# Performance work log

Measured on AMD Instinct MI355X. Metric: run time of the kernel, lower is better.

## Reference

```python
import jax, jax.numpy as jnp
import numpy as np

TAU = 2.0   # spikingjelly LIFNode default tau
VTH = 1.0   # config.vthreshold

@jax.custom_vjp
def atan_spike(x):
    # heaviside forward, ATan surrogate backward (spikingjelly surrogate.ATan, alpha=2)
    return (x >= 0).astype(x.dtype)

def _atan_fwd(x):
    return atan_spike(x), x

def _atan_bwd(x, g):
    alpha = 2.0
    return (g * (alpha / 2.0) / (1.0 + (jnp.pi / 2.0 * alpha * x) ** 2),)

atan_spike.defvjp(_atan_fwd, _atan_bwd)

def layer_norm(x, eps=1e-6):
    m = jnp.mean(x, axis=-1, keepdims=True)
    v = jnp.mean((x - m) ** 2, axis=-1, keepdims=True)
    return (x - m) * jax.lax.rsqrt(v + eps)

def time_shift(x):
    # ZeroPad2d((0,0,1,-1)): xx[:, t] = x[:, t-1], xx[:, 0] = 0
    return jnp.pad(x, ((0, 0), (1, 0), (0, 0)))[:, :-1]

def lif_multistep(x4):
    # spikingjelly LIFNode, step_mode='m', decay_input=True, hard reset to v_reset=0
    def step(v, xt):
        v = v + (xt - v) / TAU
        s = atan_spike(v - VTH)
        return v * (1.0 - s), s
    _, spikes = jax.lax.scan(step, jnp.zeros_like(x4[0]), x4)
    return spikes

def wkv(w, u, k, v):
    # RWKV-v4 numerically-stable WKV scan. w: [C] (negative), u: [C], k,v: [B,T,C]
    B, T, C = k.shape
    def step(carry, kv):
        aa, bb, pp = carry
        kt, vt = kv
        ww = u + kt
        p = jnp.maximum(pp, ww)
        e1 = jnp.exp(pp - p); e2 = jnp.exp(ww - p)
        y = (e1 * aa + e2 * vt) / (e1 * bb + e2)
        ww2 = pp + w
        p2 = jnp.maximum(ww2, kt)
        f1 = jnp.exp(ww2 - p2); f2 = jnp.exp(kt - p2)
        return (f1 * aa + f2 * vt, f1 * bb + f2, p2), y
    init = (jnp.zeros((B, C), k.dtype), jnp.zeros((B, C), k.dtype),
            jnp.full((B, C), -1e38, k.dtype))
    _, ys = jax.lax.scan(step, init, (jnp.moveaxis(k, 1, 0), jnp.moveaxis(v, 1, 0)))
    return jnp.moveaxis(ys, 0, 1)

def time_mix(h, time_decay, time_first, tmk, tmv, tmr, Wk, Wv, Wr, Wo):
    xx = time_shift(h)
    xk = h * tmk + xx * (1 - tmk)
    xv = h * tmv + xx * (1 - tmv)
    xr = h * tmr + xx * (1 - tmr)
    k = jnp.einsum('btc,oc->bto', xk, Wk)
    v = jnp.einsum('btc,oc->bto', xv, Wv)
    sr = jax.nn.sigmoid(jnp.einsum('btc,oc->bto', xr, Wr))
    y = wkv(-jnp.exp(time_decay), time_first, k, v)
    return jnp.einsum('btc,oc->bto', sr * y, Wo)

def channel_mix(h, cmk, cmr, Wck, Wcv, Wcr):
    xx = time_shift(h)
    xk = h * cmk + xx * (1 - cmk)
    xr = h * cmr + xx * (1 - cmr)
    k = jnp.square(jax.nn.relu(jnp.einsum('btc,hc->bth', xk, Wck)))
    kv = jnp.einsum('bth,ch->btc', k, Wcv)
    return jax.nn.sigmoid(jnp.einsum('btc,oc->bto', xr, Wcr)) * kv

def _forward(x, rt, time_decay, time_first, tmix_k, tmix_v, tmix_r,
             Wk, Wv, Wr, Wo, cmix_k, cmix_r, Wck, Wcv, Wcr,
             Wrm, brm, Wam, bam):
    B, P1, C = x.shape
    xc = jnp.concatenate([x, jnp.broadcast_to(rt, (B, P1, C))], axis=1)  # [B, 2*P1, C]
    att = time_mix(layer_norm(xc), time_decay, time_first,
                   tmix_k, tmix_v, tmix_r, Wk, Wv, Wr, Wo)
    att = lif_multistep(jnp.broadcast_to(att, (4,) + att.shape)).mean(0)
    xc = xc + att
    ffn = channel_mix(layer_norm(xc), cmix_k, cmix_r, Wck, Wcv, Wcr)
    ffn = lif_multistep(jnp.broadcast_to(ffn, (4,) + ffn.shape)).mean(0)
    xc = xc + ffn
    xo, rtok = xc[:, :P1], xc[:, P1:]
    r = jnp.einsum('bpc,qc->bpq', rtok, Wrm) + brm   # restruction_token_MLP [B,P1,P1]
    r = jnp.swapaxes(r, 1, 2)                        # permute(0,2,1)
    r = jnp.einsum('bpq,cq->bpc', r, Wam) + bam      # another_MLP [B,P1,C]
    return xo + xo * r

def setup_inputs() -> dict:
    key = jax.random.key(0)
    ks = jax.random.split(key, 20)
    B, P1, C = 8, 256, 1024
    H = 4 * C
    s = 0.02
    f32 = jnp.float32
    return {
        'x': jax.random.normal(ks[0], (B, P1, C), f32),
        'rt': jax.random.normal(ks[1], (1, P1, C), f32) * 0.5,
        'time_decay': jax.random.normal(ks[2], (C,), f32),
        'time_first': jax.random.normal(ks[3], (C,), f32) * 0.3,
        'tmix_k': jax.random.uniform(ks[4], (1, 1, C), f32),
        'tmix_v': jax.random.uniform(ks[5], (1, 1, C), f32),
        'tmix_r': jax.random.uniform(ks[6], (1, 1, C), f32),
        'Wk': jax.random.normal(ks[7], (C, C), f32) * s,
        'Wv': jax.random.normal(ks[8], (C, C), f32) * s,
        'Wr': jax.random.normal(ks[9], (C, C), f32) * s,
        'Wo': jax.random.normal(ks[10], (C, C), f32) * s,
        'cmix_k': jax.random.uniform(ks[11], (1, 1, C), f32),
        'cmix_r': jax.random.uniform(ks[12], (1, 1, C), f32),
        'Wck': jax.random.normal(ks[13], (H, C), f32) * s,
        'Wcv': jax.random.normal(ks[14], (C, H), f32) * s,
        'Wcr': jax.random.normal(ks[15], (C, C), f32) * s,
        'Wrm': jax.random.normal(ks[16], (P1, C), f32) * s,
        'brm': jax.random.normal(ks[17], (P1,), f32) * s,
        'Wam': jax.random.normal(ks[18], (C, P1), f32) * s,
        'bam': jax.random.normal(ks[19], (C,), f32) * s,
    }

def reference(x, rt, time_decay, time_first, tmix_k, tmix_v, tmix_r,
              Wk, Wv, Wr, Wo, cmix_k, cmix_r, Wck, Wcv, Wcr,
              Wrm, brm, Wam, bam):
    return _forward(x, rt, time_decay, time_first, tmix_k, tmix_v, tmix_r,
                    Wk, Wv, Wr, Wo, cmix_k, cmix_r, Wck, Wcv, Wcr,
                    Wrm, brm, Wam, bam)
```

## Files before the change

### kernel.cpp

```cpp
#include <hip/hip_runtime.h>
#include <hip/hip_bf16.h>
#include <math.h>
#include <stdint.h>

#define TB_ 8
#define TT_ 512
#define TC_ 1024
#define WKV_NCH 32
#define WKV_L 16

typedef __attribute__((ext_vector_type(8))) short bf16x8;
typedef __attribute__((ext_vector_type(4))) short s16x4;
typedef __attribute__((ext_vector_type(4))) float f32x4;

__device__ __forceinline__ float b2f(short u) {
  union { unsigned int i; float f; } x;
  x.i = ((unsigned int)(unsigned short)u) << 16;
  return x.f;
}
__device__ __forceinline__ short f2b(float f) {
  __hip_bfloat16 h = __float2bfloat16(f);
  return __builtin_bit_cast(short, h);
}
__device__ __forceinline__ float sigm(float x) { return 1.0f / (1.0f + expf(-x)); }

__device__ __forceinline__ float lif4(float a) {
  float v = 0.0f, acc = 0.0f;
#pragma unroll
  for (int i = 0; i < 4; ++i) {
    v += (a - v) * 0.5f;
    float s = (v >= 1.0f) ? 1.0f : 0.0f;
    acc += s;
    v *= (1.0f - s);
  }
  return acc * 0.25f;
}

__device__ __forceinline__ void gload16(const void* g, void* l) {
  __builtin_amdgcn_global_load_lds(
      (__attribute__((address_space(1))) void*)(g),
      (__attribute__((address_space(3))) void*)(l), 16, 0, 0);
}

template <int N>
__device__ __forceinline__ void waitv() {
  if constexpr (N == 0)  asm volatile("s_waitcnt vmcnt(0)" ::: "memory");
  else if constexpr (N == 2)  asm volatile("s_waitcnt vmcnt(2)" ::: "memory");
  else if constexpr (N == 4)  asm volatile("s_waitcnt vmcnt(4)" ::: "memory");
  else if constexpr (N == 6)  asm volatile("s_waitcnt vmcnt(6)" ::: "memory");
  else if constexpr (N == 8)  asm volatile("s_waitcnt vmcnt(8)" ::: "memory");
  else if constexpr (N == 12) asm volatile("s_waitcnt vmcnt(12)" ::: "memory");
  else if constexpr (N == 16) asm volatile("s_waitcnt vmcnt(16)" ::: "memory");
  else if constexpr (N == 20) asm volatile("s_waitcnt vmcnt(20)" ::: "memory");
  else if constexpr (N == 24) asm volatile("s_waitcnt vmcnt(24)" ::: "memory");
  else if constexpr (N == 28) asm volatile("s_waitcnt vmcnt(28)" ::: "memory");
  else static_assert(N == 0, "unsupported vmcnt");
}
__device__ __forceinline__ void barrier_() {
  asm volatile("s_barrier" ::: "memory");
}


__global__ __launch_bounds__(256) void ln_first(const float* __restrict__ x,
                                                const float* __restrict__ rt,
                                                float* __restrict__ xc,
                                                short* __restrict__ dst) {
  __shared__ float red[256];
  int row = blockIdx.x;
  int t = row & 511, b = row >> 9;
  const float* src = (t < 256) ? x + (int64_t)(b * 256 + t) * TC_
                               : rt + (int64_t)(t - 256) * TC_;
  float4 v = ((const float4*)src)[threadIdx.x];
  ((float4*)(xc + (int64_t)row * TC_))[threadIdx.x] = v;
  red[threadIdx.x] = v.x + v.y + v.z + v.w;
  __syncthreads();
  for (int off = 128; off > 0; off >>= 1) {
    if (threadIdx.x < off) red[threadIdx.x] += red[threadIdx.x + off];
    __syncthreads();
  }
  float mean = red[0] * (1.0f / 1024.0f);
  __syncthreads();
  float dx = v.x - mean, dy = v.y - mean, dz = v.z - mean, dw = v.w - mean;
  red[threadIdx.x] = dx * dx + dy * dy + dz * dz + dw * dw;
  __syncthreads();
  for (int off = 128; off > 0; off >>= 1) {
    if (threadIdx.x < off) red[threadIdx.x] += red[threadIdx.x + off];
    __syncthreads();
  }
  float rs = 1.0f / sqrtf(red[0] * (1.0f / 1024.0f) + 1e-6f);
  s16x4 o;
  o.x = f2b(dx * rs); o.y = f2b(dy * rs); o.z = f2b(dz * rs); o.w = f2b(dw * rs);
  *(s16x4*)(dst + (int64_t)row * TC_ + threadIdx.x * 4) = o;
}

__global__ __launch_bounds__(256) void ln_rows_b(const float* __restrict__ src,
                                                 short* __restrict__ dst) {
  __shared__ float red[256];
  int64_t row = blockIdx.x;
  float4 v = ((const float4*)(src + row * TC_))[threadIdx.x];
  red[threadIdx.x] = v.x + v.y + v.z + v.w;
  __syncthreads();
  for (int off = 128; off > 0; off >>= 1) {
    if (threadIdx.x < off) red[threadIdx.x] += red[threadIdx.x + off];
    __syncthreads();
  }
  float mean = red[0] * (1.0f / 1024.0f);
  __syncthreads();
  float dx = v.x - mean, dy = v.y - mean, dz = v.z - mean, dw = v.w - mean;
  red[threadIdx.x] = dx * dx + dy * dy + dz * dz + dw * dw;
  __syncthreads();
  for (int off = 128; off > 0; off >>= 1) {
    if (threadIdx.x < off) red[threadIdx.x] += red[threadIdx.x + off];
    __syncthreads();
  }
  float rs = 1.0f / sqrtf(red[0] * (1.0f / 1024.0f) + 1e-6f);
  s16x4 o;
  o.x = f2b(dx * rs); o.y = f2b(dy * rs); o.z = f2b(dz * rs); o.w = f2b(dw * rs);
  *(s16x4*)(dst + row * TC_ + threadIdx.x * 4) = o;
}

__global__ __launch_bounds__(256) void mix3_b(const short* __restrict__ ln,
                                              const float* __restrict__ tk,
                                              const float* __restrict__ tv,
                                              const float* __restrict__ tr,
                                              short* __restrict__ xk,
                                              short* __restrict__ xv,
                                              short* __restrict__ xr) {
  int i = blockIdx.x * 256 + threadIdx.x;
  int c8 = i & 127;
  int t = (i >> 7) & 511;
  bf16x8 h = *(const bf16x8*)(ln + (int64_t)i * 8);
  bf16x8 s = {};
  if (t > 0) s = *(const bf16x8*)(ln + (int64_t)(i - 128) * 8);
  bf16x8 ok, ov, orr;
#pragma unroll
  for (int e = 0; e < 8; ++e) {
    float hf = b2f(h[e]), sf = b2f(s[e]);
    int c = c8 * 8 + e;
    float mk = tk[c], mv = tv[c], mr = tr[c];
    ok[e] = f2b(hf * mk + sf * (1.0f - mk));
    ov[e] = f2b(hf * mv + sf * (1.0f - mv));
    orr[e] = f2b(hf * mr + sf * (1.0f - mr));
  }
  *(bf16x8*)(xk + (int64_t)i * 8) = ok;
  *(bf16x8*)(xv + (int64_t)i * 8) = ov;
  *(bf16x8*)(xr + (int64_t)i * 8) = orr;
}

__global__ __launch_bounds__(256) void mix2_b(const short* __restrict__ ln,
                                              const float* __restrict__ tk,
                                              const float* __restrict__ tr,
                                              short* __restrict__ xk,
                                              short* __restrict__ xr) {
  int i = blockIdx.x * 256 + threadIdx.x;
  int c8 = i & 127;
  int t = (i >> 7) & 511;
  bf16x8 h = *(const bf16x8*)(ln + (int64_t)i * 8);
  bf16x8 s = {};
  if (t > 0) s = *(const bf16x8*)(ln + (int64_t)(i - 128) * 8);
  bf16x8 ok, orr;
#pragma unroll
  for (int e = 0; e < 8; ++e) {
    float hf = b2f(h[e]), sf = b2f(s[e]);
    int c = c8 * 8 + e;
    float mk = tk[c], mr = tr[c];
    ok[e] = f2b(hf * mk + sf * (1.0f - mk));
    orr[e] = f2b(hf * mr + sf * (1.0f - mr));
  }
  *(bf16x8*)(xk + (int64_t)i * 8) = ok;
  *(bf16x8*)(xr + (int64_t)i * 8) = orr;
}

__global__ __launch_bounds__(256) void cvt_b(const float* __restrict__ src,
                                             short* __restrict__ dst) {
  int64_t i = (int64_t)(blockIdx.x * 256 + threadIdx.x) * 8;
  float4 a = *(const float4*)(src + i);
  float4 b = *(const float4*)(src + i + 4);
  bf16x8 o;
  o[0] = f2b(a.x); o[1] = f2b(a.y); o[2] = f2b(a.z); o[3] = f2b(a.w);
  o[4] = f2b(b.x); o[5] = f2b(b.y); o[6] = f2b(b.z); o[7] = f2b(b.w);
  *(bf16x8*)(dst + i) = o;
}

__global__ __launch_bounds__(256) void cvt_rtok(const float* __restrict__ xc,
                                                short* __restrict__ dst) {
  int i = blockIdx.x * 256 + threadIdx.x;
  int b = i >> 15;
  int rem = i & 32767;
  const float* s = xc + (int64_t)b * 524288 + 262144 + (int64_t)rem * 8;
  float4 a = *(const float4*)s;
  float4 c = *(const float4*)(s + 4);
  bf16x8 o;
  o[0] = f2b(a.x); o[1] = f2b(a.y); o[2] = f2b(a.z); o[3] = f2b(a.w);
  o[4] = f2b(c.x); o[5] = f2b(c.y); o[6] = f2b(c.z); o[7] = f2b(c.w);
  *(bf16x8*)(dst + (int64_t)i * 8) = o;
}

__global__ __launch_bounds__(256) void wkv_p1(const float* __restrict__ td,
                                              const short* __restrict__ K,
                                              const short* __restrict__ V,
                                              float* __restrict__ Ca,
                                              float* __restrict__ Da,
                                              float* __restrict__ Qa) {
  int bx = blockIdx.x;
  int ch = bx >> 5;
  int b = (bx >> 2) & 7;
  int c = (bx & 3) * 256 + threadIdx.x;
  float w = -expf(td[c]);
  float aa = 0.0f, bb = 0.0f, pp = -1e38f;
  int64_t base = ((int64_t)b * TT_ + ch * WKV_L) * TC_ + c;
#pragma unroll
  for (int t = 0; t < WKV_L; ++t) {
    int64_t o = base + (int64_t)t * TC_;
    float kt = b2f(K[o]), vt = b2f(V[o]);
    float ww2 = pp + w;
    float p2 = fmaxf(ww2, kt);
    float e1 = expf(ww2 - p2);
    float e2 = expf(kt - p2);
    aa = e1 * aa + e2 * vt;
    bb = e1 * bb + e2;
    pp = p2;
  }
  int idx = ch * 8192 + b * 1024 + c;
  Ca[idx] = aa; Da[idx] = bb; Qa[idx] = pp;
}

__global__ __launch_bounds__(256) void wkv_p2(const float* __restrict__ td,
                                              const float* __restrict__ Ca,
                                              const float* __restrict__ Da,
                                              const float* __restrict__ Qa,
                                              float* __restrict__ Aa,
                                              float* __restrict__ Ba,
                                              float* __restrict__ Pa) {
  int i = blockIdx.x * 256 + threadIdx.x;
  int c = i & (TC_ - 1);
  float wL = -expf(td[c]) * (float)WKV_L;
  float aa = 0.0f, bb = 0.0f, pp = -1e38f;
#pragma unroll 4
  for (int ch = 0; ch < WKV_NCH; ++ch) {
    int idx = ch * 8192 + i;
    Aa[idx] = aa; Ba[idx] = bb; Pa[idx] = pp;
    float ppw = pp + wL;
    float q = Qa[idx];
    float p2 = fmaxf(ppw, q);
    float ea = expf(ppw - p2);
    float eb = expf(q - p2);
    aa = aa * ea + Ca[idx] * eb;
    bb = bb * ea + Da[idx] * eb;
    pp = p2;
  }
}

__global__ __launch_bounds__(256) void wkv_p3(const float* __restrict__ td,
                                              const float* __restrict__ tf,
                                              const short* __restrict__ K,
                                              const short* __restrict__ V,
                                              const short* __restrict__ SR,
                                              short* __restrict__ SRY,
                                              const float* __restrict__ Aa,
                                              const float* __restrict__ Ba,
                                              const float* __restrict__ Pa) {
  int bx = blockIdx.x;
  int ch = bx >> 5;
  int b = (bx >> 2) & 7;
  int c = (bx & 3) * 256 + threadIdx.x;
  float w = -expf(td[c]);
  float u = tf[c];
  int idx = ch * 8192 + b * 1024 + c;
  float aa = Aa[idx], bb = Ba[idx], pp = Pa[idx];
  int64_t base = ((int64_t)b * TT_ + ch * WKV_L) * TC_ + c;
#pragma unroll
  for (int t = 0; t < WKV_L; ++t) {
    int64_t o = base + (int64_t)t * TC_;
    float kt = b2f(K[o]), vt = b2f(V[o]);
    float ww = u + kt;
    float p = fmaxf(pp, ww);
    float E1 = expf(pp - p);
    float E2 = expf(ww - p);
    float y = (E1 * aa + E2 * vt) / (E1 * bb + E2);
    SRY[o] = f2b(y * b2f(SR[o]));
    float ww2 = pp + w;
    float p2 = fmaxf(ww2, kt);
    float e1 = expf(ww2 - p2);
    float e2 = expf(kt - p2);
    aa = e1 * aa + e2 * vt;
    bb = e1 * bb + e2;
    pp = p2;
  }
}

__global__ __launch_bounds__(64) void row_sum256(const float* __restrict__ Wam,
                                                 float* __restrict__ S) {
  int c = blockIdx.x;
  int lane = threadIdx.x;
  float4 v = ((const float4*)(Wam + (int64_t)c * 256))[lane];
  float s = v.x + v.y + v.z + v.w;
  for (int off = 32; off > 0; off >>= 1) s += __shfl_down(s, off);
  if (lane == 0) S[c] = s;
}

template <int BM, int BN, int EPI, int D, int MINW>
__global__ __launch_bounds__(256, MINW) void gemm_bf16(
    const short* __restrict__ A, const short* __restrict__ B,
    void* __restrict__ Cp, int M, int N, int K,
    int64_t sA, int64_t sB, int64_t sC,
    const float* __restrict__ e0, const float* __restrict__ e1,
    const float* __restrict__ e2, const void* __restrict__ e3, int64_t sE) {
  constexpr int MF = BM / 32;
  constexpr int NF = BN / 32;
  constexpr int ASLOT = BM / 64;
  constexpr int BSLOT = BN / 64;
  constexpr int NL = ASLOT + BSLOT;
  constexpr int SBUF = (BM + BN) * 32;
  __shared__ short lds[D * SBUF];
  const int tid = threadIdx.x;

  const unsigned gx = gridDim.x, gy = gridDim.y;
  const unsigned nwg = gx * gy * gridDim.z;
  const unsigned lin = blockIdx.x + gx * (blockIdx.y + gy * blockIdx.z);
  const unsigned cs = nwg >> 3;
  const unsigned nl = (lin & 7) * cs + (lin >> 3);
  const unsigned bxs = nl % gx;
  const unsigned tmp = nl / gx;
  const unsigned bys = tmp % gy;
  const unsigned bz = tmp / gy;

  const int brow = bys * BM;
  const int bcol = bxs * BN;
  const short* Ab = A + bz * sA;
  const short* Bb = B + bz * sB;

  const int srow = ((tid >> 6) << 4) + (tid & 15);
  const int skc = ((tid >> 4) & 3) * 8;
  const short* gA[ASLOT];
  const short* gB[BSLOT];
#pragma unroll
  for (int s = 0; s < ASLOT; ++s)
    gA[s] = Ab + (int64_t)(brow + s * 64 + srow) * K + skc;
#pragma unroll
  for (int s = 0; s < BSLOT; ++s)
    gB[s] = Bb + (int64_t)(bcol + s * 64 + srow) * K + skc;

  const int lane = tid & 63, wid = tid >> 6;
  const int wr = wid >> 1, wc = wid & 1;

  f32x4 acc[MF][NF] = {};

  auto stage = [&](int buf, int k0) {
    short* d = lds + buf * SBUF;
#pragma unroll
    for (int s = 0; s < ASLOT; ++s)
      gload16(gA[s] + k0, d + s * 2048 + tid * 8);
#pragma unroll
    for (int s = 0; s < BSLOT; ++s)
      gload16(gB[s] + k0, d + BM * 32 + s * 2048 + tid * 8);
  };
  auto compute = [&](int buf) {
    const short* base = lds + buf * SBUF;
    bf16x8 af[MF], bfv[NF];
#pragma unroll
    for (int m = 0; m < MF; ++m)
      af[m] = *(const bf16x8*)(base + (wr * MF + m) * 512 + lane * 8);
#pragma unroll
    for (int n = 0; n < NF; ++n)
      bfv[n] = *(const bf16x8*)(base + BM * 32 + (wc * NF + n) * 512 + lane * 8);
#pragma unroll
    for (int m = 0; m < MF; ++m)
#pragma unroll
      for (int n = 0; n < NF; ++n)
        acc[m][n] = __builtin_amdgcn_mfma_f32_16x16x32_bf16(af[m], bfv[n],
                                                            acc[m][n], 0, 0, 0);
  };

  const int nst = K / 32;
#pragma unroll
  for (int d = 0; d < D - 1; ++d) stage(d, d * 32);
  for (int t = 0; t <= nst - D; ++t) {
    stage((t + D - 1) & (D - 1), (t + D - 1) * 32);
    waitv<(D - 1) * NL>();
    barrier_();
    compute(t & (D - 1));
    barrier_();
  }
  {
    int t = nst - D + 1;
    if constexpr (D >= 8) {
      waitv<6 * NL>(); barrier_(); compute(t & (D - 1)); barrier_(); ++t;
      waitv<5 * NL>(); barrier_(); compute(t & (D - 1)); barrier_(); ++t;
      waitv<4 * NL>(); barrier_(); compute(t & (D - 1)); barrier_(); ++t;
      waitv<3 * NL>(); barrier_(); compute(t & (D - 1)); barrier_(); ++t;
    }
    if constexpr (D >= 4) {
      waitv<2 * NL>(); barrier_(); compute(t & (D - 1)); barrier_(); ++t;
      waitv<1 * NL>(); barrier_(); compute(t & (D - 1)); barrier_(); ++t;
    }
    waitv<0>(); barrier_(); compute(t & (D - 1));
  }

  const int r0 = brow + wr * (BM / 2) + (lane >> 4) * 4;
  const int c0 = bcol + wc * (BN / 2) + (lane & 15);
#pragma unroll
  for (int m = 0; m < MF; ++m) {
#pragma unroll
    for (int j = 0; j < 4; ++j) {
      int row = r0 + m * 16 + j;
#pragma unroll
      for (int n = 0; n < NF; ++n) {
        int col = c0 + n * 16;
        float v = acc[m][n][j];
        int64_t idx = (int64_t)row * N + col;
        if (EPI == 0) {
          ((short*)Cp)[bz * sC + idx] = f2b(v);
        } else if (EPI == 1) {
          ((short*)Cp)[bz * sC + idx] = f2b(sigm(v));
        } else if (EPI == 2) {
          v = fmaxf(v, 0.0f);
          ((short*)Cp)[bz * sC + idx] = f2b(v * v);
        } else if (EPI == 3) {
          float r2 = v + e0[row] * e1[col] + e2[col];
          float xo = ((const float*)e3)[bz * sE + idx];
          ((float*)Cp)[bz * sC + idx] = xo * (1.0f + r2);
        } else if (EPI == 4) {
          float* XC = (float*)Cp;
          XC[idx] = XC[idx] + lif4(v);
        } else if (EPI == 5) {
          float* XC = (float*)Cp;
          float srr = b2f(((const short*)e3)[idx]);
          XC[idx] = XC[idx] + lif4(v * srr);
        } else if (EPI == 6) {
          ((short*)Cp)[bz * sC + idx] = f2b(bz == 2 ? sigm(v) : v);
        }
      }
    }
  }
}

extern "C" void kernel_launch(void* const* d_in, const int* in_sizes, int n_in,
                              void* d_out, int out_size, void* d_ws,
                              size_t ws_size, hipStream_t stream) {
  const float* x   = (const float*)d_in[0];
  const float* rt  = (const float*)d_in[1];
  const float* td  = (const float*)d_in[2];
  const float* tf  = (const float*)d_in[3];
  const float* tmk = (const float*)d_in[4];
  const float* tmv = (const float*)d_in[5];
  const float* tmr = (const float*)d_in[6];
  const float* Wk  = (const float*)d_in[7];
  const float* Wv  = (const float*)d_in[8];
  const float* Wr  = (const float*)d_in[9];
  const float* Wo  = (const float*)d_in[10];
  const float* cmk = (const float*)d_in[11];
  const float* cmr = (const float*)d_in[12];
  const float* Wck = (const float*)d_in[13];
  const float* Wcv = (const float*)d_in[14];
  const float* Wcr = (const float*)d_in[15];
  const float* Wrm = (const float*)d_in[16];
  const float* brm = (const float*)d_in[17];
  const float* Wam = (const float*)d_in[18];
  const float* bam = (const float*)d_in[19];
  float* out = (float*)d_out;

  const size_t MB = 1ull << 20;
  uint8_t* W8 = (uint8_t*)d_ws;
  float* XC   = (float*)(W8);
  short* L    = (short*)(W8 + 16 * MB);
  short* S1   = (short*)(W8 + 24 * MB);
  short* S2   = (short*)(W8 + 32 * MB);
  short* S3   = (short*)(W8 + 40 * MB);
  short* bWcv = (short*)(W8 + 48 * MB);
  short* bWk  = (short*)(W8 + 56 * MB);
  short* bWo  = (short*)(W8 + 62 * MB);
  short* bWcr = (short*)(W8 + 64 * MB);
  short* bWrm = (short*)(W8 + 66 * MB);
  short* bWam = (short*)(W8 + 66 * MB + 512 * 1024);
  short* KK   = (short*)(W8 + 67 * MB);
  short* VV   = (short*)(W8 + 75 * MB);
  short* RR   = (short*)(W8 + 83 * MB);
  float* Ca   = (float*)(W8 + 91 * MB);
  float* Da   = (float*)(W8 + 92 * MB);
  float* Qa   = (float*)(W8 + 93 * MB);
  float* Aa   = (float*)(W8 + 94 * MB);
  float* Ba   = (float*)(W8 + 95 * MB);
  float* Pa   = (float*)(W8 + 96 * MB);
  short* SRY  = S1;
  short* xk2  = S2;
  short* xr2  = S3;
  short* SRR  = S1;
  short* bWck = S3;
  short* H16  = KK;
  short* rtok = S2;
  short* Mt   = (short*)(W8 + 36 * MB);
  float* Sb   = (float*)(W8 + 24 * MB);

  dim3 blk(256);
  const int NV8 = 2048;

  cvt_b<<<512, blk, 0, stream>>>(Wk, bWk);
  cvt_b<<<512, blk, 0, stream>>>(Wv, bWk + 1048576);
  cvt_b<<<512, blk, 0, stream>>>(Wr, bWk + 2097152);
  cvt_b<<<512, blk, 0, stream>>>(Wo, bWo);
  cvt_b<<<512, blk, 0, stream>>>(Wcr, bWcr);
  cvt_b<<<128, blk, 0, stream>>>(Wrm, bWrm);
  cvt_b<<<128, blk, 0, stream>>>(Wam, bWam);

  ln_first<<<TB_ * TT_, blk, 0, stream>>>(x, rt, XC, L);
  mix3_b<<<NV8, blk, 0, stream>>>(L, tmk, tmv, tmr, S1, S2, S3);

  gemm_bf16<128, 128, 6, 2, 3><<<dim3(8, 32, 3), blk, 0, stream>>>(
      S1, bWk, KK, 4096, 1024, 1024, 4194304, 1048576, 4194304,
      nullptr, nullptr, nullptr, nullptr, 0);
  wkv_p1<<<WKV_NCH * TB_ * 4, blk, 0, stream>>>(td, KK, VV, Ca, Da, Qa);
  wkv_p2<<<32, blk, 0, stream>>>(td, Ca, Da, Qa, Aa, Ba, Pa);
  wkv_p3<<<WKV_NCH * TB_ * 4, blk, 0, stream>>>(td, tf, KK, VV, RR, SRY,
                                                Aa, Ba, Pa);
  gemm_bf16<128, 128, 4, 8, 1><<<dim3(8, 32, 1), blk, 0, stream>>>(
      SRY, bWo, XC, 4096, 1024, 1024, 0, 0, 0,
      nullptr, nullptr, nullptr, nullptr, 0);
  ln_rows_b<<<TB_ * TT_, blk, 0, stream>>>(XC, L);
  mix2_b<<<NV8, blk, 0, stream>>>(L, cmk, cmr, xk2, xr2);
  gemm_bf16<128, 128, 1, 8, 1><<<dim3(8, 32, 1), blk, 0, stream>>>(
      xr2, bWcr, SRR, 4096, 1024, 1024, 0, 0, 0,
      nullptr, nullptr, nullptr, nullptr, 0);
  cvt_b<<<2048, blk, 0, stream>>>(Wck, bWck);
  cvt_b<<<2048, blk, 0, stream>>>(Wcv, bWcv);
  gemm_bf16<128, 128, 2, 2, 4><<<dim3(32, 32, 1), blk, 0, stream>>>(
      xk2, bWck, H16, 4096, 4096, 1024, 0, 0, 0,
      nullptr, nullptr, nullptr, nullptr, 0);
  gemm_bf16<128, 128, 5, 8, 1><<<dim3(8, 32, 1), blk, 0, stream>>>(
      H16, bWcv, XC, 4096, 1024, 4096, 0, 0, 0,
      nullptr, nullptr, nullptr, SRR, 0);
  cvt_rtok<<<1024, blk, 0, stream>>>(XC, rtok);
  gemm_bf16<64, 64, 0, 2, 2><<<dim3(4, 4, 8), blk, 0, stream>>>(
      bWrm, rtok, Mt, 256, 256, 1024, 0, (int64_t)256 * 1024,
      (int64_t)256 * 256, nullptr, nullptr, nullptr, nullptr, 0);
  row_sum256<<<1024, dim3(64), 0, stream>>>(Wam, Sb);
  gemm_bf16<64, 64, 3, 2, 2><<<dim3(16, 4, 8), blk, 0, stream>>>(
      Mt, bWam, out, 256, 1024, 256, (int64_t)256 * 256, 0,
      (int64_t)256 * 1024, brm, Sb, bam, XC, (int64_t)512 * 1024);
}
```

Before: 355.3 us.

## Fuse weight conversions and row-sum into one kernel; retile N=1024 GEMMs

Replaces seven separate weight bf16 conversion launches, the Wcv conversion and the Wam row-sum kernel with a single cvt_all launch that dispatches on block index. This cuts launch overhead and lets the conversions run concurrently. The three 4096x1024 GEMMs switch from 128x128 tiles with 8-stage buffering to 128x64 tiles with 4 stages and two blocks per CU, doubling the grid to 512 blocks for better occupancy on the CUs. Sb moves to a new scratch offset because Wcv's conversion now happens early, and it adds vmcnt(3)/(9) wait variants for the new tile shape.

```diff
diff --git a/kernel.cpp b/kernel.cpp
--- a/kernel.cpp
+++ b/kernel.cpp
@@ -46,9 +46,11 @@
 __device__ __forceinline__ void waitv() {
   if constexpr (N == 0)  asm volatile("s_waitcnt vmcnt(0)" ::: "memory");
   else if constexpr (N == 2)  asm volatile("s_waitcnt vmcnt(2)" ::: "memory");
+  else if constexpr (N == 3)  asm volatile("s_waitcnt vmcnt(3)" ::: "memory");
   else if constexpr (N == 4)  asm volatile("s_waitcnt vmcnt(4)" ::: "memory");
   else if constexpr (N == 6)  asm volatile("s_waitcnt vmcnt(6)" ::: "memory");
   else if constexpr (N == 8)  asm volatile("s_waitcnt vmcnt(8)" ::: "memory");
+  else if constexpr (N == 9)  asm volatile("s_waitcnt vmcnt(9)" ::: "memory");
   else if constexpr (N == 12) asm volatile("s_waitcnt vmcnt(12)" ::: "memory");
   else if constexpr (N == 16) asm volatile("s_waitcnt vmcnt(16)" ::: "memory");
   else if constexpr (N == 20) asm volatile("s_waitcnt vmcnt(20)" ::: "memory");
@@ -174,6 +176,43 @@
 __global__ __launch_bounds__(256) void cvt_b(const float* __restrict__ src,
                                              short* __restrict__ dst) {
   int64_t i = (int64_t)(blockIdx.x * 256 + threadIdx.x) * 8;
+  float4 a = *(const float4*)(src + i);
+  float4 b = *(const float4*)(src + i + 4);
+  bf16x8 o;
+  o[0] = f2b(a.x); o[1] = f2b(a.y); o[2] = f2b(a.z); o[3] = f2b(a.w);
+  o[4] = f2b(b.x); o[5] = f2b(b.y); o[6] = f2b(b.z); o[7] = f2b(b.w);
+  *(bf16x8*)(dst + i) = o;
+}
+
+__global__ __launch_bounds__(256) void cvt_all(
+    const float* __restrict__ Wk, const float* __restrict__ Wv,
+    const float* __restrict__ Wr, const float* __restrict__ Wo,
+    const float* __restrict__ Wcr, const float* __restrict__ Wcv,
+    const float* __restrict__ Wrm, const float* __restrict__ Wam,
+    short* __restrict__ bWk, short* __restrict__ bWv, short* __restrict__ bWr,
+    short* __restrict__ bWo, short* __restrict__ bWcr, short* __restrict__ bWcv,
+    short* __restrict__ bWrm, short* __restrict__ bWam,
+    float* __restrict__ S) {
+  int bid = blockIdx.x;
+  if (bid >= 4864) {
+    int row = (bid - 4864) * 4 + (threadIdx.x >> 6);
+    int lane = threadIdx.x & 63;
+    float4 v = ((const float4*)(Wam + (int64_t)row * 256))[lane];
+    float s = v.x + v.y + v.z + v.w;
+    for (int off = 32; off > 0; off >>= 1) s += __shfl_down(s, off);
+    if (lane == 0) S[row] = s;
+    return;
+  }
+  const float* src; short* dst; int base;
+  if (bid < 512)       { src = Wk;  dst = bWk;  base = bid; }
+  else if (bid < 1024) { src = Wv;  dst = bWv;  base = bid - 512; }
+  else if (bid < 1536) { src = Wr;  dst = bWr;  base = bid - 1024; }
+  else if (bid < 2048) { src = Wo;  dst = bWo;  base = bid - 1536; }
+  else if (bid < 2560) { src = Wcr; dst = bWcr; base = bid - 2048; }
+  else if (bid < 4608) { src = Wcv; dst = bWcv; base = bid - 2560; }
+  else if (bid < 4736) { src = Wrm; dst = bWrm; base = bid - 4608; }
+  else                 { src = Wam; dst = bWam; base = bid - 4736; }
+  int64_t i = ((int64_t)base * 256 + threadIdx.x) * 8;
   float4 a = *(const float4*)(src + i);
   float4 b = *(const float4*)(src + i + 4);
   bf16x8 o;
@@ -287,16 +326,6 @@
     bb = e1 * bb + e2;
     pp = p2;
   }
-}
-
-__global__ __launch_bounds__(64) void row_sum256(const float* __restrict__ Wam,
-                                                 float* __restrict__ S) {
-  int c = blockIdx.x;
-  int lane = threadIdx.x;
-  float4 v = ((const float4*)(Wam + (int64_t)c * 256))[lane];
-  float s = v.x + v.y + v.z + v.w;
-  for (int off = 32; off > 0; off >>= 1) s += __shfl_down(s, off);
-  if (lane == 0) S[c] = s;
 }
 
 template <int BM, int BN, int EPI, int D, int MINW>
@@ -490,18 +519,14 @@
   short* H16  = KK;
   short* rtok = S2;
   short* Mt   = (short*)(W8 + 36 * MB);
-  float* Sb   = (float*)(W8 + 24 * MB);
+  float* Sb   = (float*)(W8 + 99 * MB);
 
   dim3 blk(256);
   const int NV8 = 2048;
 
-  cvt_b<<<512, blk, 0, stream>>>(Wk, bWk);
-  cvt_b<<<512, blk, 0, stream>>>(Wv, bWk + 1048576);
-  cvt_b<<<512, blk, 0, stream>>>(Wr, bWk + 2097152);
-  cvt_b<<<512, blk, 0, stream>>>(Wo, bWo);
-  cvt_b<<<512, blk, 0, stream>>>(Wcr, bWcr);
-  cvt_b<<<128, blk, 0, stream>>>(Wrm, bWrm);
-  cvt_b<<<128, blk, 0, stream>>>(Wam, bWam);
+  cvt_all<<<5120, blk, 0, stream>>>(Wk, Wv, Wr, Wo, Wcr, Wcv, Wrm, Wam,
+                                    bWk, bWk + 1048576, bWk + 2097152, bWo,
+                                    bWcr, bWcv, bWrm, bWam, Sb);
 
   ln_first<<<TB_ * TT_, blk, 0, stream>>>(x, rt, XC, L);
   mix3_b<<<NV8, blk, 0, stream>>>(L, tmk, tmv, tmr, S1, S2, S3);
@@ -513,27 +538,25 @@
   wkv_p2<<<32, blk, 0, stream>>>(td, Ca, Da, Qa, Aa, Ba, Pa);
   wkv_p3<<<WKV_NCH * TB_ * 4, blk, 0, stream>>>(td, tf, KK, VV, RR, SRY,
                                                 Aa, Ba, Pa);
-  gemm_bf16<128, 128, 4, 8, 1><<<dim3(8, 32, 1), blk, 0, stream>>>(
+  gemm_bf16<128, 64, 4, 4, 2><<<dim3(16, 32, 1), blk, 0, stream>>>(
       SRY, bWo, XC, 4096, 1024, 1024, 0, 0, 0,
       nullptr, nullptr, nullptr, nullptr, 0);
   ln_rows_b<<<TB_ * TT_, blk, 0, stream>>>(XC, L);
   mix2_b<<<NV8, blk, 0, stream>>>(L, cmk, cmr, xk2, xr2);
-  gemm_bf16<128, 128, 1, 8, 1><<<dim3(8, 32, 1), blk, 0, stream>>>(
+  gemm_bf16<128, 64, 1, 4, 2><<<dim3(16, 32, 1), blk, 0, stream>>>(
       xr2, bWcr, SRR, 4096, 1024, 1024, 0, 0, 0,
       nullptr, nullptr, nullptr, nullptr, 0);
   cvt_b<<<2048, blk, 0, stream>>>(Wck, bWck);
-  cvt_b<<<2048, blk, 0, stream>>>(Wcv, bWcv);
   gemm_bf16<128, 128, 2, 2, 4><<<dim3(32, 32, 1), blk, 0, stream>>>(
       xk2, bWck, H16, 4096, 4096, 1024, 0, 0, 0,
       nullptr, nullptr, nullptr, nullptr, 0);
-  gemm_bf16<128, 128, 5, 8, 1><<<dim3(8, 32, 1), blk, 0, stream>>>(
+  gemm_bf16<128, 64, 5, 4, 2><<<dim3(16, 32, 1), blk, 0, stream>>>(
       H16, bWcv, XC, 4096, 1024, 4096, 0, 0, 0,
       nullptr, nullptr, nullptr, SRR, 0);
   cvt_rtok<<<1024, blk, 0, stream>>>(XC, rtok);
   gemm_bf16<64, 64, 0, 2, 2><<<dim3(4, 4, 8), blk, 0, stream>>>(
       bWrm, rtok, Mt, 256, 256, 1024, 0, (int64_t)256 * 1024,
       (int64_t)256 * 256, nullptr, nullptr, nullptr, nullptr, 0);
-  row_sum256<<<1024, dim3(64), 0, stream>>>(Wam, Sb);
   gemm_bf16<64, 64, 3, 2, 2><<<dim3(16, 4, 8), blk, 0, stream>>>(
       Mt, bWam, out, 256, 1024, 256, (int64_t)256 * 256, 0,
       (int64_t)256 * 1024, brm, Sb, bam, XC, (int64_t)512 * 1024);
```

After: 371.8 us. 4.7% more time.
